# Performance work log

Hardware: AMD Instinct MI355X
Metric: run time of the kernel (lower is better)

## Reference

```python
import jax, jax.numpy as jnp
import numpy as np

B, S, HID, NH = 4, 4096, 1024, 16
D = HID // NH
EPS = 1e-5


def setup_inputs() -> dict:
    key = jax.random.key(0)
    ks = jax.random.split(key, 8)
    x = jax.random.normal(ks[0], (B, S, HID), dtype=jnp.float32)
    sc = 0.03  # ~xavier for 1024x1024
    Wq = jax.random.normal(ks[1], (HID, HID), dtype=jnp.float32) * sc
    Wk = jax.random.normal(ks[2], (HID, HID), dtype=jnp.float32) * sc
    Wv = jax.random.normal(ks[3], (HID, HID), dtype=jnp.float32) * sc
    Wbeta = jax.random.normal(ks[4], (HID, NH), dtype=jnp.float32) * sc
    b_beta = jnp.full((NH,), 0.9, dtype=jnp.float32)  # init.constant_(0.9)
    Wo = jax.random.normal(ks[5], (HID, HID), dtype=jnp.float32) * sc
    b_o = jnp.zeros((HID,), dtype=jnp.float32)
    ln_g = jnp.ones((HID,), dtype=jnp.float32)
    ln_b = jnp.zeros((HID,), dtype=jnp.float32)
    return {"x": x, "Wq": Wq, "Wk": Wk, "Wv": Wv, "Wbeta": Wbeta,
            "b_beta": b_beta, "Wo": Wo, "b_o": b_o, "ln_g": ln_g, "ln_b": ln_b}


def _delta_scan(q, k, v, beta):
    # q,k,v: (B,S,NH,D); beta: (B,S,NH)
    # Faithful to torch einsum 'bik,bji->bjk' with broadcast over i:
    # update[b,h,:,k'] = k_t[b,h,k'] * sum_d v_t[b,h,d]  (same row repeated)
    vsum = v.sum(-1)  # (B,S,NH)
    qs = jnp.moveaxis(q, 1, 0)       # (S,B,NH,D)
    ks_ = jnp.moveaxis(k, 1, 0)
    vs = jnp.moveaxis(vsum, 1, 0)    # (S,B,NH)
    bs = jnp.moveaxis(beta, 1, 0)    # (S,B,NH)

    def step(h, inp):
        q_t, k_t, vsum_t, beta_t = inp
        h = h * beta_t[..., None, None]
        h = h + (k_t * vsum_t[..., None])[:, :, None, :]  # broadcast over rows
        o_t = jnp.einsum('bhj,bhjk->bhk', q_t, h)
        return h, o_t

    h0 = jnp.zeros((q.shape[0], q.shape[2], D, D), dtype=q.dtype)
    _, o = jax.lax.scan(step, h0, (qs, ks_, vs, bs))
    return jnp.moveaxis(o, 0, 1)  # (B,S,NH,D)


def reference(x, Wq, Wk, Wv, Wbeta, b_beta, Wo, b_o, ln_g, ln_b):
    b, s, hid = x.shape
    residual = x
    q = (x @ Wq).reshape(b, s, NH, D)
    k = (x @ Wk).reshape(b, s, NH, D)
    v = (x @ Wv).reshape(b, s, NH, D)
    beta = jax.nn.sigmoid(x @ Wbeta + b_beta)  # (B,S,NH)
    o = _delta_scan(q, k, v, beta).reshape(b, s, hid)
    out = o @ Wo + b_o  # dropout is identity in eval
    y = residual + out
    mu = y.mean(-1, keepdims=True)
    var = ((y - mu) ** 2).mean(-1, keepdims=True)
    return ln_g * (y - mu) * jax.lax.rsqrt(var + EPS) + ln_b
```

## Files before the change

### kernel.cpp

```cpp
#include <hip/hip_runtime.h>
#include <hip/hip_bf16.h>

typedef unsigned short u16;
typedef unsigned int   u32;
typedef u32 __attribute__((address_space(1))) gas_u32;
typedef u32 __attribute__((address_space(3))) las_u32;
typedef __bf16 bf16x8 __attribute__((ext_vector_type(8)));
typedef float  f32x4  __attribute__((ext_vector_type(4)));

constexpr int BATCH = 4, SEQ = 4096, HID = 1024, NH = 16, DH = 64;
constexpr int M  = BATCH * SEQ;
constexpr int KD = HID;

__device__ __forceinline__ u16 f2bf(float f) {
  __hip_bfloat16 h = __float2bfloat16(f);
  u16 u; __builtin_memcpy(&u, &h, 2); return u;
}
__device__ __forceinline__ float bf2f(u16 u) {
  u32 x = ((u32)u) << 16; float f; __builtin_memcpy(&f, &x, 4); return f;
}


__global__ __launch_bounds__(256) void transpose_cast(const float* __restrict__ Wk,
                                                      const float* __restrict__ Wo,
                                                      u16* __restrict__ WkT,
                                                      u16* __restrict__ WoT) {
  __shared__ float tile[32][33];
  const float* src = blockIdx.z ? Wo : Wk;
  u16* dst = blockIdx.z ? WoT : WkT;
  int bx = blockIdx.x * 32, by = blockIdx.y * 32;
  int tx = threadIdx.x & 31, ty = threadIdx.x >> 5;
#pragma unroll
  for (int i = 0; i < 4; i++)
    tile[ty + i * 8][tx] = src[(size_t)(by + ty + i * 8) * HID + bx + tx];
  __syncthreads();
#pragma unroll
  for (int i = 0; i < 4; i++)
    dst[(size_t)(bx + ty + i * 8) * HID + by + tx] = f2bf(tile[tx][ty + i * 8]);
}

__global__ __launch_bounds__(256) void build_wsum(const float* __restrict__ Wq,
                                                  const float* __restrict__ Wv,
                                                  const float* __restrict__ Wbeta,
                                                  u16* __restrict__ WsT) {
  int tid = blockIdx.x * 256 + threadIdx.x;
  int c = tid >> 10, kk = tid & 1023;
  float s = 0.f;
  if (c < 16)      { for (int d = 0; d < DH; d++) s += Wq[(size_t)kk * HID + c * DH + d]; }
  else if (c < 32) { for (int d = 0; d < DH; d++) s += Wv[(size_t)kk * HID + (c - 16) * DH + d]; }
  else if (c < 48) { s = Wbeta[(size_t)kk * NH + (c - 32)]; }
  WsT[(size_t)c * HID + kk] = f2bf(s);
}

__global__ __launch_bounds__(256) void skinny_part(
    const float* __restrict__ x, const u16* __restrict__ Bt,
    float* __restrict__ pq, float* __restrict__ pv, float* __restrict__ pb,
    u16* __restrict__ xb) {
  constexpr int BM = 64, BK = 64, KC = 256;
  __shared__ u16 As[BM * BK];
  __shared__ u16 Bs[64 * BK];
  const int tid = threadIdx.x, wave = tid >> 6, lane = tid & 63;
  const int bm = (int)blockIdx.x >> 2, kc = (int)blockIdx.x & 3;
  const int k0 = kc * KC;
  const int r16 = lane & 15, hi = lane >> 4;
  const int rsub = lane >> 3, csub = (lane & 7) * 8;
  f32x4 acc[4] = {};
  const float* Ab = x + (size_t)bm * BM * KD;
  u16* xbb = xb + (size_t)bm * BM * KD;

  for (int kt = k0; kt < k0 + KC; kt += BK) {
#pragma unroll
    for (int i = 0; i < 2; i++) {
      int slot = wave * 2 + i;
      const u16* g = Bt + (size_t)(slot * 8 + rsub) * KD + kt + csub;
      __builtin_amdgcn_global_load_lds((const gas_u32*)g, (las_u32*)(Bs + slot * 512), 16, 0, 0);
    }
#pragma unroll
    for (int p = 0; p < 2; p++) {
      const int row = p * 32 + (tid >> 3);
      const int c8 = (tid & 7) * 8;
      const float4 u0 = *(const float4*)(Ab + (size_t)row * KD + kt + c8);
      const float4 u1 = *(const float4*)(Ab + (size_t)row * KD + kt + c8 + 4);
      uint4 w;
      w.x = (u32)f2bf(u0.x) | ((u32)f2bf(u0.y) << 16);
      w.y = (u32)f2bf(u0.z) | ((u32)f2bf(u0.w) << 16);
      w.z = (u32)f2bf(u1.x) | ((u32)f2bf(u1.y) << 16);
      w.w = (u32)f2bf(u1.z) | ((u32)f2bf(u1.w) << 16);
      *(uint4*)(As + row * BK + c8) = w;
      *(uint4*)(xbb + (size_t)row * KD + kt + c8) = w;
    }
    __syncthreads();
#pragma unroll
    for (int kk = 0; kk < 2; kk++) {
      bf16x8 af = *(const bf16x8*)(As + (wave * 16 + r16) * BK + kk * 32 + hi * 8);
#pragma unroll
      for (int fn = 0; fn < 4; fn++) {
        bf16x8 bfr = *(const bf16x8*)(Bs + (fn * 16 + r16) * BK + kk * 32 + hi * 8);
        acc[fn] = __builtin_amdgcn_mfma_f32_16x16x32_bf16(af, bfr, acc[fn], 0, 0, 0);
      }
    }
    __syncthreads();
  }

  const size_t kcoff = (size_t)kc * 64 * SEQ;
#pragma unroll
  for (int fn = 0; fn < 4; fn++) {
    const int col = fn * 16 + r16;
#pragma unroll
    for (int j = 0; j < 4; j++) {
      const int row = bm * BM + wave * 16 + hi * 4 + j;
      const int b = row >> 12, t = row & 4095;
      float v = acc[fn][j];
      if (col < 16)      pq[kcoff + ((size_t)(b * 16 + col)) * SEQ + t] = v;
      else if (col < 32) pv[kcoff + ((size_t)(b * 16 + col - 16)) * SEQ + t] = v;
      else if (col < 48) pb[kcoff + ((size_t)(b * 16 + col - 32)) * SEQ + t] = v;
    }
  }
}


__device__ __forceinline__ void stage_quarter(const u16* __restrict__ Gk,
                                              int q, u16* lds_tile, int tid, int wave) {
  const int row = q * 64 + (tid >> 3);
  const int s = tid & 7;
  const u16* g = Gk + (size_t)row * KD + (size_t)((s ^ (row & 7)) << 3);
  u16* l = lds_tile + q * 4096 + wave * 512;
  __builtin_amdgcn_global_load_lds((const gas_u32*)g, (las_u32*)l, 16, 0, 0);
}

__device__ __forceinline__ const bf16x8* lds_frag(const u16* lds_tile, int row, int cg) {
  return (const bf16x8*)(lds_tile + ((size_t)row << 6) + (size_t)((cg ^ (row & 7)) << 3));
}

template <int EPI>
__global__ __launch_bounds__(512) void gemm256(
    const u16* __restrict__ A, const u16* __restrict__ Bt, int N,
    u16* __restrict__ Cb, const u16* __restrict__ xres, const float* __restrict__ bias) {
  constexpr int BK = 64, NT = KD / BK;
  __shared__ u16 lds[2][2][16384];
  const int tid = threadIdx.x, wave = tid >> 6, lane = tid & 63;
  const int wm = wave >> 2, wn = wave & 3;
  const int r16 = lane & 15, hi = lane >> 4;
  const int bid = (int)blockIdx.x;
  const int bm = (bid & 7) + 8 * (bid >> 5);
  const int bn = (bid >> 3) & 3;
  const u16* Abase = A + (size_t)bm * 256 * KD;
  const u16* Bbase = Bt + (size_t)bn * 256 * KD;

  f32x4 acc[8][4] = {};

  {
    u16* la0 = &lds[0][0][0]; u16* lb0 = &lds[0][1][0];
    stage_quarter(Abase, 0, la0, tid, wave);
    stage_quarter(Abase, 2, la0, tid, wave);
    stage_quarter(Bbase, 0, lb0, tid, wave);
    stage_quarter(Bbase, 1, lb0, tid, wave);
    stage_quarter(Bbase, 2, lb0, tid, wave);
    stage_quarter(Bbase, 3, lb0, tid, wave);
    stage_quarter(Abase, 1, la0, tid, wave);
    stage_quarter(Abase, 3, la0, tid, wave);
    const u16* A1 = Abase + BK; const u16* B1 = Bbase + BK;
    u16* la1 = &lds[1][0][0]; u16* lb1 = &lds[1][1][0];
    stage_quarter(A1, 0, la1, tid, wave);
    stage_quarter(A1, 2, la1, tid, wave);
    stage_quarter(B1, 0, lb1, tid, wave);
    stage_quarter(B1, 1, lb1, tid, wave);
    stage_quarter(B1, 2, lb1, tid, wave);
    stage_quarter(B1, 3, lb1, tid, wave);
  }
  asm volatile("s_waitcnt vmcnt(8)" ::: "memory");
  __builtin_amdgcn_s_barrier();

  for (int kt = 0; kt < NT; ++kt) {
    const int cur = kt & 1;
    const u16* la = &lds[cur][0][0];
    const u16* lb = &lds[cur][1][0];

    if (kt + 1 < NT) {
      const u16* An1 = Abase + (kt + 1) * BK;
      u16* na = &lds[cur ^ 1][0][0];
      stage_quarter(An1, 1, na, tid, wave);
      stage_quarter(An1, 3, na, tid, wave);
    }
    bf16x8 bF[4][2], aF0[4][2];
#pragma unroll
    for (int kk = 0; kk < 2; ++kk) {
#pragma unroll
      for (int f = 0; f < 4; ++f)
        aF0[f][kk] = *lds_frag(la, wm * 128 + f * 16 + r16, kk * 4 + hi);
#pragma unroll
      for (int g = 0; g < 4; ++g)
        bF[g][kk] = *lds_frag(lb, wn * 64 + g * 16 + r16, kk * 4 + hi);
    }
    __builtin_amdgcn_s_setprio(1);
#pragma unroll
    for (int kk = 0; kk < 2; ++kk)
#pragma unroll
      for (int f = 0; f < 4; ++f)
#pragma unroll
        for (int g = 0; g < 4; ++g)
          acc[f][g] = __builtin_amdgcn_mfma_f32_16x16x32_bf16(
              aF0[f][kk], bF[g][kk], acc[f][g], 0, 0, 0);
    __builtin_amdgcn_s_setprio(0);
    if (kt < NT - 1)      { asm volatile("s_waitcnt vmcnt(8)" ::: "memory"); }
    else                  { asm volatile("s_waitcnt vmcnt(0)" ::: "memory"); }
    __builtin_amdgcn_s_barrier();

    if (kt + 2 < NT) {
      const u16* An2 = Abase + (kt + 2) * BK;
      const u16* Bn2 = Bbase + (kt + 2) * BK;
      u16* ca = &lds[cur][0][0];
      u16* cb = &lds[cur][1][0];
      stage_quarter(An2, 0, ca, tid, wave);
      stage_quarter(An2, 2, ca, tid, wave);
      stage_quarter(Bn2, 0, cb, tid, wave);
      stage_quarter(Bn2, 1, cb, tid, wave);
      stage_quarter(Bn2, 2, cb, tid, wave);
      stage_quarter(Bn2, 3, cb, tid, wave);
    }
    bf16x8 aF1[4][2];
#pragma unroll
    for (int kk = 0; kk < 2; ++kk)
#pragma unroll
      for (int f = 0; f < 4; ++f)
        aF1[f][kk] = *lds_frag(la, wm * 128 + 64 + f * 16 + r16, kk * 4 + hi);
    __builtin_amdgcn_s_setprio(1);
#pragma unroll
    for (int kk = 0; kk < 2; ++kk)
#pragma unroll
      for (int f = 0; f < 4; ++f)
#pragma unroll
        for (int g = 0; g < 4; ++g)
          acc[4 + f][g] = __builtin_amdgcn_mfma_f32_16x16x32_bf16(
              aF1[f][kk], bF[g][kk], acc[4 + f][g], 0, 0, 0);
    __builtin_amdgcn_s_setprio(0);
    if (kt < NT - 2)      { asm volatile("s_waitcnt vmcnt(8)" ::: "memory"); __builtin_amdgcn_s_barrier(); }
    else if (kt == NT - 2){ asm volatile("s_waitcnt vmcnt(2)" ::: "memory"); __builtin_amdgcn_s_barrier(); }
  }

#pragma unroll
  for (int fm = 0; fm < 8; ++fm) {
#pragma unroll
    for (int fn = 0; fn < 4; ++fn) {
      const int col = bn * 256 + wn * 64 + fn * 16 + r16;
#pragma unroll
      for (int j = 0; j < 4; ++j) {
        const int row = bm * 256 + wm * 128 + fm * 16 + hi * 4 + j;
        float v = acc[fm][fn][j];
        if constexpr (EPI == 2) v += bf2f(xres[(size_t)row * N + col]) + bias[col];
        Cb[(size_t)row * N + col] = f2bf(v);
      }
    }
  }
}


__global__ __launch_bounds__(256) void scan_chunks(const u16* __restrict__ kbuf,
                                                   const float* __restrict__ pv,
                                                   const float* __restrict__ pb,
                                                   const float* __restrict__ bbeta,
                                                   float* __restrict__ Pbuf,
                                                   float* __restrict__ Rloc) {
  constexpr size_t STR = (size_t)64 * SEQ;
  const int wave = threadIdx.x >> 6, lane = threadIdx.x & 63;
  const int gid = blockIdx.x * 4 + wave;
  const int seq = gid >> 6, chunk = gid & 63;
  const int b = seq >> 4, h = seq & 15;
  const int t0 = chunk * 64;
  const size_t idx = (size_t)seq * SEQ + t0 + lane;
  const float zb = pb[idx] + pb[idx + STR] + pb[idx + 2 * STR] + pb[idx + 3 * STR] + bbeta[h];
  const float bet = 1.f / (1.f + __expf(-zb));
  const float vs  = pv[idx] + pv[idx + STR] + pv[idx + 2 * STR] + pv[idx + 3 * STR];
  const u16* kp = kbuf + ((size_t)(b * SEQ + t0)) * HID + h * DH + lane;
  float r = 0.f, P = 1.f;
#pragma unroll
  for (int tt = 0; tt < 64; tt += 8) {
    u16 kr[8];
#pragma unroll
    for (int j = 0; j < 8; j++) kr[j] = kp[(size_t)(tt + j) * HID];
#pragma unroll
    for (int j = 0; j < 8; j++) {
      float bt = __shfl(bet, tt + j);
      float vt = __shfl(vs, tt + j);
      r = fmaf(r, bt, bf2f(kr[j]) * vt);
      P *= bt;
    }
  }
  Rloc[(size_t)gid * 64 + lane] = r;
  if (lane == 0) Pbuf[gid] = P;
}

__global__ __launch_bounds__(64) void scan_prefix(const float* __restrict__ Pbuf,
                                                  const float* __restrict__ Rloc,
                                                  float* __restrict__ Rin) {
  const int seq = blockIdx.x, lane = threadIdx.x;
  const float* pp = Pbuf + seq * 64;
  const float* rl = Rloc + (size_t)seq * 64 * 64 + lane;
  float* ri = Rin + (size_t)seq * 64 * 64 + lane;
  float rin = 0.f;
#pragma unroll
  for (int c0 = 0; c0 < 64; c0 += 8) {
    float P[8], L[8];
#pragma unroll
    for (int j = 0; j < 8; j++) { P[j] = pp[c0 + j]; L[j] = rl[(size_t)(c0 + j) * 64]; }
#pragma unroll
    for (int j = 0; j < 8; j++) {
      ri[(size_t)(c0 + j) * 64] = rin;
      rin = fmaf(P[j], rin, L[j]);
    }
  }
}

__global__ __launch_bounds__(256) void scan_apply(const u16* __restrict__ kbuf,
                                                  const float* __restrict__ pq,
                                                  const float* __restrict__ pv,
                                                  const float* __restrict__ pb,
                                                  const float* __restrict__ bbeta,
                                                  const float* __restrict__ Rin,
                                                  u16* __restrict__ obuf) {
  constexpr size_t STR = (size_t)64 * SEQ;
  const int wave = threadIdx.x >> 6, lane = threadIdx.x & 63;
  const int gid = blockIdx.x * 4 + wave;
  const int seq = gid >> 6, chunk = gid & 63;
  const int b = seq >> 4, h = seq & 15;
  const int t0 = chunk * 64;
  const size_t idx = (size_t)seq * SEQ + t0 + lane;
  const float zb = pb[idx] + pb[idx + STR] + pb[idx + 2 * STR] + pb[idx + 3 * STR] + bbeta[h];
  const float bet = 1.f / (1.f + __expf(-zb));
  const float vs  = pv[idx] + pv[idx + STR] + pv[idx + 2 * STR] + pv[idx + 3 * STR];
  const float qs  = pq[idx] + pq[idx + STR] + pq[idx + 2 * STR] + pq[idx + 3 * STR];
  const u16* kp = kbuf + ((size_t)(b * SEQ + t0)) * HID + h * DH + lane;
  u16* op = obuf + ((size_t)(b * SEQ + t0)) * HID + h * DH + lane;
  float r = Rin[(size_t)gid * 64 + lane];
#pragma unroll
  for (int tt = 0; tt < 64; tt += 8) {
    u16 kr[8];
#pragma unroll
    for (int j = 0; j < 8; j++) kr[j] = kp[(size_t)(tt + j) * HID];
#pragma unroll
    for (int j = 0; j < 8; j++) {
      float bt = __shfl(bet, tt + j);
      float vt = __shfl(vs, tt + j);
      float qt = __shfl(qs, tt + j);
      r = fmaf(r, bt, bf2f(kr[j]) * vt);
      op[(size_t)(tt + j) * HID] = f2bf(qt * r);
    }
  }
}

__global__ __launch_bounds__(256) void ln_kernel(const u16* __restrict__ y,
                                                 const float* __restrict__ g,
                                                 const float* __restrict__ bt,
                                                 float* __restrict__ out) {
  const int row = blockIdx.x;
  const u16* yr = y + (size_t)row * HID;
  const int t = threadIdx.x;
  ushort4 u = *(const ushort4*)(yr + t * 4);
  float v0 = bf2f(u.x), v1 = bf2f(u.y), v2 = bf2f(u.z), v3 = bf2f(u.w);
  float s  = v0 + v1 + v2 + v3;
  float ss = v0 * v0 + v1 * v1 + v2 * v2 + v3 * v3;
#pragma unroll
  for (int m = 1; m < 64; m <<= 1) { s += __shfl_xor(s, m); ss += __shfl_xor(ss, m); }
  __shared__ float red[8];
  const int wave = t >> 6, lane = t & 63;
  if (lane == 0) { red[wave] = s; red[4 + wave] = ss; }
  __syncthreads();
  float st  = red[0] + red[1] + red[2] + red[3];
  float sst = red[4] + red[5] + red[6] + red[7];
  float mu  = st * (1.f / 1024.f);
  float var = sst * (1.f / 1024.f) - mu * mu;
  float inv = rsqrtf(var + 1e-5f);
  const int c = t * 4;
  float4 o;
  o.x = g[c + 0] * ((v0 - mu) * inv) + bt[c + 0];
  o.y = g[c + 1] * ((v1 - mu) * inv) + bt[c + 1];
  o.z = g[c + 2] * ((v2 - mu) * inv) + bt[c + 2];
  o.w = g[c + 3] * ((v3 - mu) * inv) + bt[c + 3];
  *(float4*)(out + (size_t)row * HID + c) = o;
}

extern "C" void kernel_launch(void* const* d_in, const int* in_sizes, int n_in,
                              void* d_out, int out_size, void* d_ws, size_t ws_size,
                              hipStream_t stream) {
  const float* x     = (const float*)d_in[0];
  const float* Wq    = (const float*)d_in[1];
  const float* Wk    = (const float*)d_in[2];
  const float* Wv    = (const float*)d_in[3];
  const float* Wbeta = (const float*)d_in[4];
  const float* bbeta = (const float*)d_in[5];
  const float* Wo    = (const float*)d_in[6];
  const float* b_o   = (const float*)d_in[7];
  const float* ln_g  = (const float*)d_in[8];
  const float* ln_b  = (const float*)d_in[9];
  float* out = (float*)d_out;

  char* ws = (char*)d_ws;
  size_t off = 0;
  auto alloc = [&](size_t bytes) {
    char* p = ws + off; off += (bytes + 255) & ~(size_t)255; return p;
  };
  u16* xb   = (u16*)alloc((size_t)M * HID * 2);
  u16* kbuf = (u16*)alloc((size_t)M * HID * 2);
  u16* obuf = (u16*)alloc((size_t)M * HID * 2);
  u16* WkT  = (u16*)alloc((size_t)HID * HID * 2);
  u16* WoT  = (u16*)alloc((size_t)HID * HID * 2);
  u16* WsT  = (u16*)alloc((size_t)64 * HID * 2);
  float* pq = (float*)alloc((size_t)4 * 64 * SEQ * 4);
  float* pv = (float*)alloc((size_t)4 * 64 * SEQ * 4);
  float* pb = (float*)alloc((size_t)4 * 64 * SEQ * 4);
  float* Pbuf = (float*)alloc((size_t)4096 * 4);
  float* Rloc = (float*)alloc((size_t)4096 * 64 * 4);
  float* Rin  = (float*)alloc((size_t)4096 * 64 * 4);
  u16* ybuf = kbuf;

  transpose_cast<<<dim3(32, 32, 2), 256, 0, stream>>>(Wk, Wo, WkT, WoT);
  build_wsum<<<256, 256, 0, stream>>>(Wq, Wv, Wbeta, WsT);

  skinny_part<<<(M / 64) * 4, 256, 0, stream>>>(x, WsT, pq, pv, pb, xb);

  gemm256<0><<<(M / 256) * (HID / 256), 512, 0, stream>>>(
      xb, WkT, HID, kbuf, nullptr, nullptr);

  scan_chunks<<<1024, 256, 0, stream>>>(kbuf, pv, pb, bbeta, Pbuf, Rloc);
  scan_prefix<<<64, 64, 0, stream>>>(Pbuf, Rloc, Rin);
  scan_apply<<<1024, 256, 0, stream>>>(kbuf, pq, pv, pb, bbeta, Rin, obuf);

  gemm256<2><<<(M / 256) * (HID / 256), 512, 0, stream>>>(
      obuf, WoT, HID, ybuf, xb, b_o);

  ln_kernel<<<M, 256, 0, stream>>>(ybuf, ln_g, ln_b, out);
}
```

Before: 150.7 us.

## Double GEMM block to 1024 threads with 2x8 wave grid and paired staging

The 256x256 GEMM tile now runs with 16 waves in a 2x8 grid instead of 8 waves in 2x4, so each wave computes 128x32 and holds half the accumulators. Staging is rewritten so each load instruction covers two quarter-tiles across 1024 threads. The prefetch schedule moves from a two-stage lookahead to a single next-tile double buffer, with waitcnts adjusted to match. The aim is more waves for latency hiding and lower register pressure. The cost is more LDS fragment reads per MFMA, and a shallower prefetch that may expose global load latency.

```diff
diff --git a/kernel.cpp b/kernel.cpp
--- a/kernel.cpp
+++ b/kernel.cpp
@@ -119,12 +119,14 @@
 }
 
 
-__device__ __forceinline__ void stage_quarter(const u16* __restrict__ Gk,
-                                              int q, u16* lds_tile, int tid, int wave) {
-  const int row = q * 64 + (tid >> 3);
-  const int s = tid & 7;
+__device__ __forceinline__ void stage_pair(const u16* __restrict__ Gk,
+                                           int qa, int qb, u16* lds_tile, int tid) {
+  const int q = (tid >> 9) ? qb : qa;
+  const int t9 = tid & 511;
+  const int row = q * 64 + (t9 >> 3);
+  const int s = t9 & 7;
   const u16* g = Gk + (size_t)row * KD + (size_t)((s ^ (row & 7)) << 3);
-  u16* l = lds_tile + q * 4096 + wave * 512;
+  u16* l = lds_tile + q * 4096 + ((tid >> 6) & 7) * 512;
   __builtin_amdgcn_global_load_lds((const gas_u32*)g, (las_u32*)l, 16, 0, 0);
 }
 
@@ -133,13 +135,13 @@
 }
 
 template <int EPI>
-__global__ __launch_bounds__(512) void gemm256(
+__global__ __launch_bounds__(1024, 4) void gemm256(
     const u16* __restrict__ A, const u16* __restrict__ Bt, int N,
     u16* __restrict__ Cb, const u16* __restrict__ xres, const float* __restrict__ bias) {
   constexpr int BK = 64, NT = KD / BK;
   __shared__ u16 lds[2][2][16384];
   const int tid = threadIdx.x, wave = tid >> 6, lane = tid & 63;
-  const int wm = wave >> 2, wn = wave & 3;
+  const int wm = wave >> 3, wn = wave & 7;
   const int r16 = lane & 15, hi = lane >> 4;
   const int bid = (int)blockIdx.x;
   const int bm = (bid & 7) + 8 * (bid >> 5);
@@ -147,50 +149,38 @@
   const u16* Abase = A + (size_t)bm * 256 * KD;
   const u16* Bbase = Bt + (size_t)bn * 256 * KD;
 
-  f32x4 acc[8][4] = {};
+  f32x4 acc[8][2] = {};
 
   {
-    u16* la0 = &lds[0][0][0]; u16* lb0 = &lds[0][1][0];
-    stage_quarter(Abase, 0, la0, tid, wave);
-    stage_quarter(Abase, 2, la0, tid, wave);
-    stage_quarter(Bbase, 0, lb0, tid, wave);
-    stage_quarter(Bbase, 1, lb0, tid, wave);
-    stage_quarter(Bbase, 2, lb0, tid, wave);
-    stage_quarter(Bbase, 3, lb0, tid, wave);
-    stage_quarter(Abase, 1, la0, tid, wave);
-    stage_quarter(Abase, 3, la0, tid, wave);
-    const u16* A1 = Abase + BK; const u16* B1 = Bbase + BK;
-    u16* la1 = &lds[1][0][0]; u16* lb1 = &lds[1][1][0];
-    stage_quarter(A1, 0, la1, tid, wave);
-    stage_quarter(A1, 2, la1, tid, wave);
-    stage_quarter(B1, 0, lb1, tid, wave);
-    stage_quarter(B1, 1, lb1, tid, wave);
-    stage_quarter(B1, 2, lb1, tid, wave);
-    stage_quarter(B1, 3, lb1, tid, wave);
-  }
-  asm volatile("s_waitcnt vmcnt(8)" ::: "memory");
+    u16* la = &lds[0][0][0]; u16* lb = &lds[0][1][0];
+    stage_pair(Abase, 0, 2, la, tid);
+    stage_pair(Bbase, 0, 1, lb, tid);
+    stage_pair(Bbase, 2, 3, lb, tid);
+    stage_pair(Abase, 1, 3, la, tid);
+  }
+  asm volatile("s_waitcnt vmcnt(1)" ::: "memory");
   __builtin_amdgcn_s_barrier();
 
   for (int kt = 0; kt < NT; ++kt) {
     const int cur = kt & 1;
     const u16* la = &lds[cur][0][0];
     const u16* lb = &lds[cur][1][0];
-
-    if (kt + 1 < NT) {
-      const u16* An1 = Abase + (kt + 1) * BK;
-      u16* na = &lds[cur ^ 1][0][0];
-      stage_quarter(An1, 1, na, tid, wave);
-      stage_quarter(An1, 3, na, tid, wave);
-    }
-    bf16x8 bF[4][2], aF0[4][2];
+    u16* na = &lds[cur ^ 1][0][0];
+    u16* nb = &lds[cur ^ 1][1][0];
+    const bool hasNext = (kt + 1 < NT);
+    const u16* An = Abase + (kt + 1) * BK;
+    const u16* Bn = Bbase + (kt + 1) * BK;
+
+    if (hasNext) stage_pair(An, 0, 2, na, tid);
+    bf16x8 bF[2][2], aF[4][2];
 #pragma unroll
     for (int kk = 0; kk < 2; ++kk) {
 #pragma unroll
       for (int f = 0; f < 4; ++f)
-        aF0[f][kk] = *lds_frag(la, wm * 128 + f * 16 + r16, kk * 4 + hi);
-#pragma unroll
-      for (int g = 0; g < 4; ++g)
-        bF[g][kk] = *lds_frag(lb, wn * 64 + g * 16 + r16, kk * 4 + hi);
+        aF[f][kk] = *lds_frag(la, wm * 128 + f * 16 + r16, kk * 4 + hi);
+#pragma unroll
+      for (int g = 0; g < 2; ++g)
+        bF[g][kk] = *lds_frag(lb, wn * 32 + g * 16 + r16, kk * 4 + hi);
     }
     __builtin_amdgcn_s_setprio(1);
 #pragma unroll
@@ -198,51 +188,43 @@
 #pragma unroll
       for (int f = 0; f < 4; ++f)
 #pragma unroll
-        for (int g = 0; g < 4; ++g)
+        for (int g = 0; g < 2; ++g)
           acc[f][g] = __builtin_amdgcn_mfma_f32_16x16x32_bf16(
-              aF0[f][kk], bF[g][kk], acc[f][g], 0, 0, 0);
+              aF[f][kk], bF[g][kk], acc[f][g], 0, 0, 0);
     __builtin_amdgcn_s_setprio(0);
-    if (kt < NT - 1)      { asm volatile("s_waitcnt vmcnt(8)" ::: "memory"); }
-    else                  { asm volatile("s_waitcnt vmcnt(0)" ::: "memory"); }
+    if (hasNext) { asm volatile("s_waitcnt vmcnt(1)" ::: "memory"); }
+    else         { asm volatile("s_waitcnt vmcnt(0)" ::: "memory"); }
     __builtin_amdgcn_s_barrier();
 
-    if (kt + 2 < NT) {
-      const u16* An2 = Abase + (kt + 2) * BK;
-      const u16* Bn2 = Bbase + (kt + 2) * BK;
-      u16* ca = &lds[cur][0][0];
-      u16* cb = &lds[cur][1][0];
-      stage_quarter(An2, 0, ca, tid, wave);
-      stage_quarter(An2, 2, ca, tid, wave);
-      stage_quarter(Bn2, 0, cb, tid, wave);
-      stage_quarter(Bn2, 1, cb, tid, wave);
-      stage_quarter(Bn2, 2, cb, tid, wave);
-      stage_quarter(Bn2, 3, cb, tid, wave);
-    }
-    bf16x8 aF1[4][2];
+    if (hasNext) { stage_pair(Bn, 0, 1, nb, tid); stage_pair(Bn, 2, 3, nb, tid); }
+    bf16x8 aG[4][2];
 #pragma unroll
     for (int kk = 0; kk < 2; ++kk)
 #pragma unroll
       for (int f = 0; f < 4; ++f)
-        aF1[f][kk] = *lds_frag(la, wm * 128 + 64 + f * 16 + r16, kk * 4 + hi);
+        aG[f][kk] = *lds_frag(la, wm * 128 + 64 + f * 16 + r16, kk * 4 + hi);
+    if (hasNext) stage_pair(An, 1, 3, na, tid);
     __builtin_amdgcn_s_setprio(1);
 #pragma unroll
     for (int kk = 0; kk < 2; ++kk)
 #pragma unroll
       for (int f = 0; f < 4; ++f)
 #pragma unroll
-        for (int g = 0; g < 4; ++g)
+        for (int g = 0; g < 2; ++g)
           acc[4 + f][g] = __builtin_amdgcn_mfma_f32_16x16x32_bf16(
-              aF1[f][kk], bF[g][kk], acc[4 + f][g], 0, 0, 0);
+              aG[f][kk], bF[g][kk], acc[4 + f][g], 0, 0, 0);
     __builtin_amdgcn_s_setprio(0);
-    if (kt < NT - 2)      { asm volatile("s_waitcnt vmcnt(8)" ::: "memory"); __builtin_amdgcn_s_barrier(); }
-    else if (kt == NT - 2){ asm volatile("s_waitcnt vmcnt(2)" ::: "memory"); __builtin_amdgcn_s_barrier(); }
+    if (hasNext) {
+      asm volatile("s_waitcnt vmcnt(1)" ::: "memory");
+      __builtin_amdgcn_s_barrier();
+    }
   }
 
 #pragma unroll
   for (int fm = 0; fm < 8; ++fm) {
 #pragma unroll
-    for (int fn = 0; fn < 4; ++fn) {
-      const int col = bn * 256 + wn * 64 + fn * 16 + r16;
+    for (int fn = 0; fn < 2; ++fn) {
+      const int col = bn * 256 + wn * 32 + fn * 16 + r16;
 #pragma unroll
       for (int j = 0; j < 4; ++j) {
         const int row = bm * 256 + wm * 128 + fm * 16 + hi * 4 + j;
@@ -418,14 +400,14 @@
 
   skinny_part<<<(M / 64) * 4, 256, 0, stream>>>(x, WsT, pq, pv, pb, xb);
 
-  gemm256<0><<<(M / 256) * (HID / 256), 512, 0, stream>>>(
+  gemm256<0><<<(M / 256) * (HID / 256), 1024, 0, stream>>>(
       xb, WkT, HID, kbuf, nullptr, nullptr);
 
   scan_chunks<<<1024, 256, 0, stream>>>(kbuf, pv, pb, bbeta, Pbuf, Rloc);
   scan_prefix<<<64, 64, 0, stream>>>(Pbuf, Rloc, Rin);
   scan_apply<<<1024, 256, 0, stream>>>(kbuf, pq, pv, pb, bbeta, Rin, obuf);
 
-  gemm256<2><<<(M / 256) * (HID / 256), 512, 0, stream>>>(
+  gemm256<2><<<(M / 256) * (HID / 256), 1024, 0, stream>>>(
       obuf, WoT, HID, ybuf, xb, b_o);
 
   ln_kernel<<<M, 256, 0, stream>>>(ybuf, ln_g, ln_b, out);
```

Measured after the change: 168.6 us. +11.8%, slower.
